# Kernel tuning notes

Hardware: AMD Instinct MI355X
Metric: run time of the kernel (lower is better)

The kernel has to match this reference:

```python
import jax, jax.numpy as jnp
import numpy as np
import math

EPS = 1e-5  # torch BatchNorm2d default eps
EXPANSION_RATE = 2


def _bn_train(x, gamma, beta):
    # BatchNorm2d in training mode: biased batch statistics over (B, H, W)
    mu = jnp.mean(x, axis=(0, 2, 3), keepdims=True)
    var = jnp.var(x, axis=(0, 2, 3), keepdims=True)
    xn = (x - mu) * jax.lax.rsqrt(var + EPS)
    return gamma[None, :, None, None] * xn + beta[None, :, None, None]


def _conv1x1(x, w, b):
    # w: [O, C]  (1x1 conv kernel squeezed), b: [O]
    return jnp.einsum('bchw,oc->bohw', x, w) + b[None, :, None, None]


def _lsgc(x, w_diff, b_diff, g_bn, be_bn, w_in, b_in, g_ibn, be_ibn,
          w_mr, b_mr, g_mbn, be_mbn):
    B, C, H, W = x.shape
    bit_depth = max(math.ceil(math.log2(H)), math.ceil(math.log2(W)))
    steps = [EXPANSION_RATE * 2 ** (n - 1) for n in range(1, bit_depth + 1)]

    fmax = None
    for step in steps:
        for axis, size in ((3, W), (2, H)):
            s = step % size
            for sgn in (1, -1):  # forward / backward rolls
                shifted = jnp.roll(x, sgn * s, axis=axis) if s else x
                d = x - shifted
                fmax = d if fmax is None else jnp.maximum(fmax, d)

    x_diff = _bn_train(_conv1x1(fmax, w_diff, b_diff), g_bn, be_bn)
    x_proc = _bn_train(_conv1x1(x, w_in, b_in), g_ibn, be_ibn)

    # MRConv: concat -> 1x1 conv -> BN -> GELU (exact) -> residual add
    x_cat = jnp.concatenate([x_proc, x_diff], axis=1)
    h = _bn_train(_conv1x1(x_cat, w_mr, b_mr), g_mbn, be_mbn)
    h = jax.nn.gelu(h, approximate=False)
    return x_proc + h


def setup_inputs() -> dict:
    key = jax.random.key(0)
    ks = jax.random.split(key, 8)
    B, C_in, C_out, H, W = 32, 128, 128, 64, 64

    def kaiming(k, o, i):
        return jax.random.normal(k, (o, i), jnp.float32) * np.sqrt(2.0 / i)

    return {
        'x': jax.random.normal(ks[0], (B, C_in, H, W), jnp.float32),
        'w_diff': kaiming(ks[1], C_out, C_in),
        'b_diff': jnp.zeros((C_out,), jnp.float32),
        'g_bn': jnp.ones((C_out,), jnp.float32),
        'be_bn': jnp.zeros((C_out,), jnp.float32),
        'w_in': kaiming(ks[2], C_out, C_in),
        'b_in': jnp.zeros((C_out,), jnp.float32),
        'g_ibn': jnp.ones((C_out,), jnp.float32),
        'be_ibn': jnp.zeros((C_out,), jnp.float32),
        'w_mr': kaiming(ks[3], C_out, 2 * C_out),
        'b_mr': jnp.zeros((C_out,), jnp.float32),
        'g_mbn': jnp.ones((C_out,), jnp.float32),
        'be_mbn': jnp.zeros((C_out,), jnp.float32),
    }


def reference(x, w_diff, b_diff, g_bn, be_bn, w_in, b_in, g_ibn, be_ibn,
              w_mr, b_mr, g_mbn, be_mbn):
    return _lsgc(x, w_diff, b_diff, g_bn, be_bn, w_in, b_in, g_ibn, be_ibn,
                 w_mr, b_mr, g_mbn, be_mbn)
```

## Files before the change

### kernel.cpp

```cpp
#include <hip/hip_runtime.h>
#include <math.h>


#define INV_NPIX (1.0f / 131072.0f)
#define EPS 1e-5f
#define KP 66
#define T1 4
#define T2 2

typedef __attribute__((ext_vector_type(8))) short s16x8;
typedef __attribute__((ext_vector_type(4))) float f32x4;

__device__ __forceinline__ uint32_t bf16_rne(float v) {
  uint32_t x = __float_as_uint(v);
  return (x + 0x7fffu + ((x >> 16) & 1u)) >> 16;
}
__device__ __forceinline__ uint32_t pack_hl(float v) {
  uint32_t h = bf16_rne(v);
  float lo = v - __uint_as_float(h << 16);
  return h | (bf16_rne(lo) << 16);
}
__device__ __forceinline__ float bf_lo(uint32_t d) {
  return __uint_as_float(d << 16);
}
__device__ __forceinline__ float bf_hi(uint32_t d) {
  return __uint_as_float(d & 0xffff0000u);
}
__device__ __forceinline__ float4 fmin4(float4 a, float4 b) {
  return make_float4(fminf(a.x, b.x), fminf(a.y, b.y), fminf(a.z, b.z),
                     fminf(a.w, b.w));
}

__global__ __launch_bounds__(256) void stencil_prep_kernel(
    const float* __restrict__ x, uint32_t* __restrict__ xp,
    uint32_t* __restrict__ fp, const float* __restrict__ w_in,
    const float* __restrict__ w_diff, unsigned short* __restrict__ wInH,
    unsigned short* __restrict__ wInL, unsigned short* __restrict__ wDfH,
    unsigned short* __restrict__ wDfL) {
  __shared__ float4 pA[1024];
  __shared__ float4 pB[1024];
  if (blockIdx.x >= 2048) {
    const int t = (blockIdx.x - 2048) * 256 + threadIdx.x;
    const int e = t & 16383;
    const float* w = (t < 16384) ? w_in : w_diff;
    unsigned short* aH = (t < 16384) ? wInH : wDfH;
    unsigned short* aL = (t < 16384) ? wInL : wDfL;
    const int j = e & 7, l = (e >> 3) & 63, mt = (e >> 9) & 7, kc = e >> 12;
    const int m = mt * 16 + (l & 15);
    const int k = kc * 32 + ((l >> 4) << 3) + j;
    const uint32_t p = pack_hl(w[m * 128 + k]);
    aH[e] = (unsigned short)(p & 0xffffu);
    aL[e] = (unsigned short)(p >> 16);
    return;
  }
  const int b = blockIdx.x >> 6;
  const int cp = blockIdx.x & 63;
  const float4* xa = (const float4*)x + (size_t)(b * 128 + 2 * cp) * 1024;
  const float4* xb = xa + 1024;
  float4 sA[4], sB[4];
#pragma unroll
  for (int i = 0; i < 4; ++i) {
    const int u = threadIdx.x + i * 256;
    sA[i] = xa[u];
    sB[i] = xb[u];
    pA[u] = sA[i];
    pB[u] = sB[i];
  }
  __syncthreads();
  const size_t obase = (size_t)(b * 64 + cp) * 1024;
#pragma unroll
  for (int i = 0; i < 4; ++i) {
    const int u = threadIdx.x + i * 256;
    const int h = u >> 4, wu = u & 15;
    const int row = u & ~15;
    float4 mA, mB;
    {
      const float4 A = sA[i];
      const float4 L = pA[row | ((wu + 15) & 15)];
      const float4 R = pA[row | ((wu + 1) & 15)];
      float4 m = fmin4(A, fmin4(L, R));
      m = fmin4(m, make_float4(A.z, A.w, R.x, R.y));
      m = fmin4(m, make_float4(L.z, L.w, A.x, A.y));
      m = fmin4(m, pA[row | ((wu + 2) & 15)]);
      m = fmin4(m, pA[row | ((wu + 14) & 15)]);
      m = fmin4(m, pA[row | ((wu + 4) & 15)]);
      m = fmin4(m, pA[row | ((wu + 12) & 15)]);
      m = fmin4(m, pA[row | ((wu + 8) & 15)]);
      m = fmin4(m, pA[(((h + 2) & 63) << 4) | wu]);
      m = fmin4(m, pA[(((h + 62) & 63) << 4) | wu]);
      m = fmin4(m, pA[(((h + 4) & 63) << 4) | wu]);
      m = fmin4(m, pA[(((h + 60) & 63) << 4) | wu]);
      m = fmin4(m, pA[(((h + 8) & 63) << 4) | wu]);
      m = fmin4(m, pA[(((h + 56) & 63) << 4) | wu]);
      m = fmin4(m, pA[(((h + 16) & 63) << 4) | wu]);
      m = fmin4(m, pA[(((h + 48) & 63) << 4) | wu]);
      m = fmin4(m, pA[(((h + 32) & 63) << 4) | wu]);
      mA = m;
    }
    {
      const float4 A = sB[i];
      const float4 L = pB[row | ((wu + 15) & 15)];
      const float4 R = pB[row | ((wu + 1) & 15)];
      float4 m = fmin4(A, fmin4(L, R));
      m = fmin4(m, make_float4(A.z, A.w, R.x, R.y));
      m = fmin4(m, make_float4(L.z, L.w, A.x, A.y));
      m = fmin4(m, pB[row | ((wu + 2) & 15)]);
      m = fmin4(m, pB[row | ((wu + 14) & 15)]);
      m = fmin4(m, pB[row | ((wu + 4) & 15)]);
      m = fmin4(m, pB[row | ((wu + 12) & 15)]);
      m = fmin4(m, pB[row | ((wu + 8) & 15)]);
      m = fmin4(m, pB[(((h + 2) & 63) << 4) | wu]);
      m = fmin4(m, pB[(((h + 62) & 63) << 4) | wu]);
      m = fmin4(m, pB[(((h + 4) & 63) << 4) | wu]);
      m = fmin4(m, pB[(((h + 60) & 63) << 4) | wu]);
      m = fmin4(m, pB[(((h + 8) & 63) << 4) | wu]);
      m = fmin4(m, pB[(((h + 56) & 63) << 4) | wu]);
      m = fmin4(m, pB[(((h + 16) & 63) << 4) | wu]);
      m = fmin4(m, pB[(((h + 48) & 63) << 4) | wu]);
      m = fmin4(m, pB[(((h + 32) & 63) << 4) | wu]);
      mB = m;
    }
    uint4 px, pf;
    px.x = bf16_rne(sA[i].x) | (bf16_rne(sB[i].x) << 16);
    px.y = bf16_rne(sA[i].y) | (bf16_rne(sB[i].y) << 16);
    px.z = bf16_rne(sA[i].z) | (bf16_rne(sB[i].z) << 16);
    px.w = bf16_rne(sA[i].w) | (bf16_rne(sB[i].w) << 16);
    pf.x = bf16_rne(sA[i].x - mA.x) | (bf16_rne(sB[i].x - mB.x) << 16);
    pf.y = bf16_rne(sA[i].y - mA.y) | (bf16_rne(sB[i].y - mB.y) << 16);
    pf.z = bf16_rne(sA[i].z - mA.z) | (bf16_rne(sB[i].z - mB.z) << 16);
    pf.w = bf16_rne(sA[i].w - mA.w) | (bf16_rne(sB[i].w - mB.w) << 16);
    ((uint4*)xp)[obase + u] = px;
    ((uint4*)fp)[obase + u] = pf;
  }
}

__device__ __forceinline__ void cwrite_stats(
    const f32x4 (&acc)[2][4], uint32_t* __restrict__ outp,
    float* __restrict__ pS, float* __restrict__ pQ, const int bx, const int b,
    const int hw0, const int wave, const int q, const int ln) {
#pragma unroll
  for (int mt2 = 0; mt2 < 2; ++mt2) {
    float sa[4] = {0.f, 0.f, 0.f, 0.f};
    float sq[4] = {0.f, 0.f, 0.f, 0.f};
#pragma unroll
    for (int nt = 0; nt < 4; ++nt) {
#pragma unroll
      for (int rp = 0; rp < 2; ++rp) {
        const float v0 = acc[mt2][nt][2 * rp];
        const float v1 = acc[mt2][nt][2 * rp + 1];
        const int m2 = (wave * 2 + mt2) * 8 + q * 2 + rp;
        outp[((size_t)(b * 64 + m2)) * 4096 + hw0 + nt * 16 + ln] =
            bf16_rne(v0) | (bf16_rne(v1) << 16);
        sa[2 * rp] += v0;
        sq[2 * rp] += v0 * v0;
        sa[2 * rp + 1] += v1;
        sq[2 * rp + 1] += v1 * v1;
      }
    }
#pragma unroll
    for (int off = 1; off < 16; off <<= 1) {
#pragma unroll
      for (int r = 0; r < 4; ++r) {
        sa[r] += __shfl_xor(sa[r], off);
        sq[r] += __shfl_xor(sq[r], off);
      }
    }
    if (ln == 0) {
#pragma unroll
      for (int r = 0; r < 4; ++r) {
        const int m = (wave * 2 + mt2) * 16 + q * 4 + r;
        pS[bx * 128 + m] = sa[r];
        pQ[bx * 128 + m] = sq[r];
      }
    }
  }
}

template <int T>
__device__ __forceinline__ void gemm1_persist(
    const unsigned short* __restrict__ AH, const unsigned short* __restrict__ AL,
    const uint32_t* __restrict__ B0, uint32_t* __restrict__ outp,
    float* __restrict__ pS, float* __restrict__ pQ, const int p,
    uint32_t* Bs) {
  const int tid = threadIdx.x;
  const int lane = tid & 63;
  const int wave = tid >> 6;
  const int sk2 = tid >> 4;
  const int sn4 = (tid & 15) << 2;
  const int q = lane >> 4;
  const int ln = lane & 15;

  uint4 ld[4];
  {
    const int bx0 = p * T;
    const int b = bx0 >> 6, hw0 = (bx0 & 63) << 6;
#pragma unroll
    for (int c = 0; c < 4; ++c)
      ld[c] = *(const uint4*)&B0[((size_t)(b * 64 + c * 16 + sk2)) * 4096 +
                                 hw0 + sn4];
  }

#pragma unroll
  for (int t = 0; t < T; ++t) {
    const int bx = p * T + t;
    const int b = bx >> 6, hw0 = (bx & 63) << 6;
    uint32_t* buf = Bs + (t & 1) * (64 * KP);

#pragma unroll
    for (int c = 0; c < 4; ++c)
      *(uint4*)&buf[(c * 16 + sk2) * KP + sn4] = ld[c];

    s16x8 ah[2][2], al[2][2];
#pragma unroll
    for (int mt2 = 0; mt2 < 2; ++mt2) {
      const size_t off = ((size_t)((wave * 2 + mt2) * 64 + lane)) << 3;
      ah[0][mt2] = *(const s16x8*)(AH + off);
      al[0][mt2] = *(const s16x8*)(AL + off);
    }
    __syncthreads();

    if (t + 1 < T) {
      const int bn = bx + 1;
      const int b2 = bn >> 6, hw2 = (bn & 63) << 6;
#pragma unroll
      for (int c = 0; c < 4; ++c)
        ld[c] = *(const uint4*)&B0[((size_t)(b2 * 64 + c * 16 + sk2)) * 4096 +
                                   hw2 + sn4];
    }

    f32x4 acc[2][4];
#pragma unroll
    for (int i = 0; i < 2; ++i)
#pragma unroll
      for (int j = 0; j < 4; ++j) acc[i][j] = (f32x4)(0.0f);

#pragma unroll
    for (int kc = 0; kc < 4; ++kc) {
      if (kc < 3) {
#pragma unroll
        for (int mt2 = 0; mt2 < 2; ++mt2) {
          const size_t off =
              ((size_t)(((kc + 1) * 8 + wave * 2 + mt2) * 64 + lane)) << 3;
          ah[(kc + 1) & 1][mt2] = *(const s16x8*)(AH + off);
          al[(kc + 1) & 1][mt2] = *(const s16x8*)(AL + off);
        }
      }
#pragma unroll
      for (int nt = 0; nt < 4; ++nt) {
        union { uint32_t u[4]; s16x8 s; } bb;
#pragma unroll
        for (int j = 0; j < 4; ++j)
          bb.u[j] = buf[(kc * 16 + q * 4 + j) * KP + nt * 16 + ln];
#pragma unroll
        for (int mt2 = 0; mt2 < 2; ++mt2) {
          acc[mt2][nt] = __builtin_amdgcn_mfma_f32_16x16x32_bf16(
              ah[kc & 1][mt2], bb.s, acc[mt2][nt], 0, 0, 0);
          acc[mt2][nt] = __builtin_amdgcn_mfma_f32_16x16x32_bf16(
              al[kc & 1][mt2], bb.s, acc[mt2][nt], 0, 0, 0);
        }
      }
    }

    cwrite_stats(acc, outp, pS, pQ, bx, b, hw0, wave, q, ln);
  }
}

__global__ __launch_bounds__(256) void gemm1_dual(
    const unsigned short* __restrict__ AH1, const unsigned short* __restrict__ AL1,
    const uint32_t* __restrict__ XP, uint32_t* __restrict__ out1,
    float* __restrict__ sv1, float* __restrict__ sq1,
    const unsigned short* __restrict__ AH2, const unsigned short* __restrict__ AL2,
    const uint32_t* __restrict__ FP, uint32_t* __restrict__ out2,
    float* __restrict__ sv2, float* __restrict__ sq2) {
  __shared__ uint32_t Bs[2 * 64 * KP];
  const int p = blockIdx.x & 511;
  if (blockIdx.x < 512)
    gemm1_persist<T1>(AH1, AL1, XP, out1, sv1, sq1, p, Bs);
  else
    gemm1_persist<T1>(AH2, AL2, FP, out2, sv2, sq2, p, Bs);
}

template <int T>
__device__ __forceinline__ void gemm2_persist(
    const unsigned short* __restrict__ AH, const unsigned short* __restrict__ AL,
    const uint32_t* __restrict__ B0, const uint32_t* __restrict__ B1,
    uint32_t* __restrict__ outp, float* __restrict__ pS,
    float* __restrict__ pQ, const int p, uint32_t* Bs) {
  const int tid = threadIdx.x;
  const int lane = tid & 63;
  const int wave = tid >> 6;
  const int sk2 = tid >> 4;
  const int sn4 = (tid & 15) << 2;
  const int q = lane >> 4;
  const int ln = lane & 15;

  uint4 ld[4];
  {
    const int bx0 = p * T;
    const int b = bx0 >> 6, hw0 = (bx0 & 63) << 6;
#pragma unroll
    for (int c = 0; c < 4; ++c)
      ld[c] = *(const uint4*)&B0[((size_t)(b * 64 + c * 16 + sk2)) * 4096 +
                                 hw0 + sn4];
  }

#pragma unroll
  for (int t = 0; t < T; ++t) {
    const int bx = p * T + t;
    const int b = bx >> 6, hw0 = (bx & 63) << 6;

    f32x4 acc[2][4];
#pragma unroll
    for (int i = 0; i < 2; ++i)
#pragma unroll
      for (int j = 0; j < 4; ++j) acc[i][j] = (f32x4)(0.0f);

    s16x8 ah[2][2], al[2][2];

    {
      uint32_t* buf = Bs;
#pragma unroll
      for (int c = 0; c < 4; ++c)
        *(uint4*)&buf[(c * 16 + sk2) * KP + sn4] = ld[c];
#pragma unroll
      for (int mt2 = 0; mt2 < 2; ++mt2) {
        const size_t off = ((size_t)((wave * 2 + mt2) * 64 + lane)) << 3;
        ah[0][mt2] = *(const s16x8*)(AH + off);
        al[0][mt2] = *(const s16x8*)(AL + off);
      }
      __syncthreads();
#pragma unroll
      for (int c = 0; c < 4; ++c)
        ld[c] = *(const uint4*)&B1[((size_t)(b * 64 + c * 16 + sk2)) * 4096 +
                                   hw0 + sn4];
#pragma unroll
      for (int kc = 0; kc < 4; ++kc) {
        if (kc < 3) {
#pragma unroll
          for (int mt2 = 0; mt2 < 2; ++mt2) {
            const size_t off =
                ((size_t)(((kc + 1) * 8 + wave * 2 + mt2) * 64 + lane)) << 3;
            ah[(kc + 1) & 1][mt2] = *(const s16x8*)(AH + off);
            al[(kc + 1) & 1][mt2] = *(const s16x8*)(AL + off);
          }
        }
#pragma unroll
        for (int nt = 0; nt < 4; ++nt) {
          union { uint32_t u[4]; s16x8 s; } bb;
#pragma unroll
          for (int j = 0; j < 4; ++j)
            bb.u[j] = buf[(kc * 16 + q * 4 + j) * KP + nt * 16 + ln];
#pragma unroll
          for (int mt2 = 0; mt2 < 2; ++mt2) {
            acc[mt2][nt] = __builtin_amdgcn_mfma_f32_16x16x32_bf16(
                ah[kc & 1][mt2], bb.s, acc[mt2][nt], 0, 0, 0);
            acc[mt2][nt] = __builtin_amdgcn_mfma_f32_16x16x32_bf16(
                al[kc & 1][mt2], bb.s, acc[mt2][nt], 0, 0, 0);
          }
        }
      }
    }

    {
      uint32_t* buf = Bs + 64 * KP;
#pragma unroll
      for (int c = 0; c < 4; ++c)
        *(uint4*)&buf[(c * 16 + sk2) * KP + sn4] = ld[c];
#pragma unroll
      for (int mt2 = 0; mt2 < 2; ++mt2) {
        const size_t off =
            ((size_t)((4 * 8 + wave * 2 + mt2) * 64 + lane)) << 3;
        ah[0][mt2] = *(const s16x8*)(AH + off);
        al[0][mt2] = *(const s16x8*)(AL + off);
      }
      __syncthreads();
      if (t + 1 < T) {
        const int bn = bx + 1;
        const int b2 = bn >> 6, hw2 = (bn & 63) << 6;
#pragma unroll
        for (int c = 0; c < 4; ++c)
          ld[c] = *(const uint4*)&B0[((size_t)(b2 * 64 + c * 16 + sk2)) * 4096 +
                                     hw2 + sn4];
      }
#pragma unroll
      for (int kc = 4; kc < 8; ++kc) {
        if (kc < 7) {
#pragma unroll
          for (int mt2 = 0; mt2 < 2; ++mt2) {
            const size_t off =
                ((size_t)(((kc + 1) * 8 + wave * 2 + mt2) * 64 + lane)) << 3;
            ah[(kc + 1) & 1][mt2] = *(const s16x8*)(AH + off);
            al[(kc + 1) & 1][mt2] = *(const s16x8*)(AL + off);
          }
        }
#pragma unroll
        for (int nt = 0; nt < 4; ++nt) {
          union { uint32_t u[4]; s16x8 s; } bb;
#pragma unroll
          for (int j = 0; j < 4; ++j)
            bb.u[j] = buf[((kc - 4) * 16 + q * 4 + j) * KP + nt * 16 + ln];
#pragma unroll
          for (int mt2 = 0; mt2 < 2; ++mt2) {
            acc[mt2][nt] = __builtin_amdgcn_mfma_f32_16x16x32_bf16(
                ah[kc & 1][mt2], bb.s, acc[mt2][nt], 0, 0, 0);
            acc[mt2][nt] = __builtin_amdgcn_mfma_f32_16x16x32_bf16(
                al[kc & 1][mt2], bb.s, acc[mt2][nt], 0, 0, 0);
          }
        }
      }
    }

    cwrite_stats(acc, outp, pS, pQ, bx, b, hw0, wave, q, ln);
  }
}

__global__ __launch_bounds__(256) void gemm2_kernel(
    const unsigned short* __restrict__ AH, const unsigned short* __restrict__ AL,
    const uint32_t* __restrict__ B0, const uint32_t* __restrict__ B1,
    uint32_t* __restrict__ outp, float* __restrict__ sv,
    float* __restrict__ sq) {
  __shared__ uint32_t Bs[2 * 64 * KP];
  gemm2_persist<T2>(AH, AL, B0, B1, outp, sv, sq, blockIdx.x, Bs);
}

__global__ __launch_bounds__(256) void reduce_kernel(
    const float* __restrict__ P, float* __restrict__ p2) {
  const int a = blockIdx.x >> 4, g = blockIdx.x & 15;
  const int c = threadIdx.x & 127, h = threadIdx.x >> 7;
  const float* src = P + ((size_t)(a * 2048 + g * 128 + h * 64)) * 128 + c;
  float s0 = 0.f, s1 = 0.f, s2 = 0.f, s3 = 0.f;
#pragma unroll
  for (int j = 0; j < 64; j += 4) {
    s0 += src[(j + 0) * 128];
    s1 += src[(j + 1) * 128];
    s2 += src[(j + 2) * 128];
    s3 += src[(j + 3) * 128];
  }
  __shared__ float sm[256];
  sm[threadIdx.x] = (s0 + s1) + (s2 + s3);
  __syncthreads();
  if (h == 0) p2[(a * 16 + g) * 128 + c] = sm[c] + sm[128 + c];
}

__global__ __launch_bounds__(256) void finalize1_kernel(
    const float* __restrict__ p2, const float* __restrict__ g_ibn,
    const float* __restrict__ be_ibn, const float* __restrict__ g_bn,
    const float* __restrict__ w_mr, float* __restrict__ a_in,
    float* __restrict__ d_in, unsigned short* __restrict__ wEffH,
    unsigned short* __restrict__ wEffL) {
  __shared__ float sa[256];
  const int t = threadIdx.x;
  if (t < 128) {
    float s = 0.f, qq = 0.f;
#pragma unroll
    for (int g = 0; g < 16; ++g) {
      s += p2[g * 128 + t];
      qq += p2[(16 + g) * 128 + t];
    }
    const float mu = s * INV_NPIX;
    const float var = fmaxf(qq * INV_NPIX - mu * mu, 0.f);
    const float a = g_ibn[t] * rsqrtf(var + EPS);
    if (blockIdx.x == 0) {
      a_in[t] = a;
      d_in[t] = be_ibn[t] - mu * a;
    }
    sa[t] = a;
  } else {
    const int c = t - 128;
    float s = 0.f, qq = 0.f;
#pragma unroll
    for (int g = 0; g < 16; ++g) {
      s += p2[(32 + g) * 128 + c];
      qq += p2[(48 + g) * 128 + c];
    }
    const float mu = s * INV_NPIX;
    const float var = fmaxf(qq * INV_NPIX - mu * mu, 0.f);
    sa[t] = g_bn[c] * rsqrtf(var + EPS);
  }
  __syncthreads();
  const int e = blockIdx.x * 256 + t;
  const int j = e & 7, l = (e >> 3) & 63, mt = (e >> 9) & 7, kc = e >> 12;
  const int m = mt * 16 + (l & 15);
  const int k = kc * 32 + ((l >> 4) << 3) + j;
  const uint32_t p = pack_hl(w_mr[m * 256 + k] * sa[k]);
  wEffH[e] = (unsigned short)(p & 0xffffu);
  wEffL[e] = (unsigned short)(p >> 16);
}

__global__ __launch_bounds__(128) void finalize2_kernel(
    const float* __restrict__ p2h, const float* __restrict__ g_mbn,
    const float* __restrict__ be_mbn, float* __restrict__ a_m,
    float* __restrict__ d_m) {
  const int t = threadIdx.x;
  float s = 0.f, qq = 0.f;
#pragma unroll
  for (int g = 0; g < 16; ++g) {
    s += p2h[g * 128 + t];
    qq += p2h[(16 + g) * 128 + t];
  }
  const float mu = s * INV_NPIX;
  const float var = fmaxf(qq * INV_NPIX - mu * mu, 0.f);
  const float a = g_mbn[t] * rsqrtf(var + EPS);
  a_m[t] = a;
  d_m[t] = be_mbn[t] - mu * a;
}

__device__ __forceinline__ float gelu_exact(float z) {
  return 0.5f * z * (1.0f + erff(z * 0.70710678118654752f));
}

__global__ __launch_bounds__(256) void epilogue_kernel(
    const uint32_t* __restrict__ yp, const uint32_t* __restrict__ hp,
    const float* __restrict__ a_in, const float* __restrict__ d_in,
    const float* __restrict__ a_m, const float* __restrict__ d_m,
    float* __restrict__ out) {
  const size_t i = (size_t)blockIdx.x * 256 + threadIdx.x;
  const int cp = (int)((i >> 10) & 63);
  const int b = (int)(i >> 16);
  const int c0 = 2 * cp, c1 = 2 * cp + 1;
  const uint4 yv = ((const uint4*)yp)[i];
  const uint4 hv = ((const uint4*)hp)[i];
  const float a0 = a_in[c0], d0 = d_in[c0], m0 = a_m[c0], e0 = d_m[c0];
  const float a1 = a_in[c1], d1 = d_in[c1], m1 = a_m[c1], e1 = d_m[c1];
  float4 o0, o1;
  o0.x = fmaf(a0, bf_lo(yv.x), d0) + gelu_exact(fmaf(m0, bf_lo(hv.x), e0));
  o0.y = fmaf(a0, bf_lo(yv.y), d0) + gelu_exact(fmaf(m0, bf_lo(hv.y), e0));
  o0.z = fmaf(a0, bf_lo(yv.z), d0) + gelu_exact(fmaf(m0, bf_lo(hv.z), e0));
  o0.w = fmaf(a0, bf_lo(yv.w), d0) + gelu_exact(fmaf(m0, bf_lo(hv.w), e0));
  o1.x = fmaf(a1, bf_hi(yv.x), d1) + gelu_exact(fmaf(m1, bf_hi(hv.x), e1));
  o1.y = fmaf(a1, bf_hi(yv.y), d1) + gelu_exact(fmaf(m1, bf_hi(hv.y), e1));
  o1.z = fmaf(a1, bf_hi(yv.z), d1) + gelu_exact(fmaf(m1, bf_hi(hv.z), e1));
  o1.w = fmaf(a1, bf_hi(yv.w), d1) + gelu_exact(fmaf(m1, bf_hi(hv.w), e1));
  const size_t u = i & 1023;
  ((float4*)out)[(size_t)(b * 128 + c0) * 1024 + u] = o0;
  ((float4*)out)[(size_t)(b * 128 + c1) * 1024 + u] = o1;
}

extern "C" void kernel_launch(void* const* d_in, const int* in_sizes, int n_in,
                              void* d_out, int out_size, void* d_ws,
                              size_t ws_size, hipStream_t stream) {
  const float* x = (const float*)d_in[0];
  const float* w_diff = (const float*)d_in[1];
  const float* g_bn = (const float*)d_in[3];
  const float* w_in = (const float*)d_in[5];
  const float* g_ibn = (const float*)d_in[7];
  const float* be_ibn = (const float*)d_in[8];
  const float* w_mr = (const float*)d_in[9];
  const float* g_mbn = (const float*)d_in[11];
  const float* be_mbn = (const float*)d_in[12];
  float* out = (float*)d_out;

  const size_t PD = (size_t)8388608;
  uint32_t* ws = (uint32_t*)d_ws;
  uint32_t* xp = ws;
  uint32_t* fpx = ws + PD;
  uint32_t* ypIn = ws + 2 * PD;
  uint32_t* ypDf = ws + 3 * PD;
  uint32_t* hp = ws + 4 * PD;
  float* st = (float*)(ws + 5 * PD);
  float* p2 = st;
  float* p2h = st + 8192;
  float* a_in = st + 12288, *dinc = st + 12416;
  float* a_m = st + 12544, *d_m = st + 12672;
  unsigned short* fr = (unsigned short*)(st + 12800);
  unsigned short* wInH = fr;
  unsigned short* wInL = fr + 16384;
  unsigned short* wDfH = fr + 32768;
  unsigned short* wDfL = fr + 49152;
  unsigned short* wEffH = fr + 65536;
  unsigned short* wEffL = fr + 98304;
  float* g1p = (float*)(ws + 4 * PD);
  float* g2p = (float*)ws;

  stencil_prep_kernel<<<2176, 256, 0, stream>>>(x, xp, fpx, w_in, w_diff,
                                                wInH, wInL, wDfH, wDfL);
  gemm1_dual<<<1024, 256, 0, stream>>>(wInH, wInL, xp, ypIn, g1p,
                                       g1p + 262144, wDfH, wDfL, fpx, ypDf,
                                       g1p + 524288, g1p + 786432);
  reduce_kernel<<<64, 256, 0, stream>>>(g1p, p2);
  finalize1_kernel<<<128, 256, 0, stream>>>(p2, g_ibn, be_ibn, g_bn, w_mr,
                                            a_in, dinc, wEffH, wEffL);
  gemm2_kernel<<<1024, 256, 0, stream>>>(wEffH, wEffL, ypIn, ypDf, hp, g2p,
                                         g2p + 262144);
  reduce_kernel<<<32, 256, 0, stream>>>(g2p, p2h);
  finalize2_kernel<<<1, 128, 0, stream>>>(p2h, g_mbn, be_mbn, a_m, d_m);
  epilogue_kernel<<<8192, 256, 0, stream>>>(ypIn, hp, a_in, dinc, a_m, d_m,
                                            out);
}
```

Measured before the change: 253.4 us.

## Stage GEMM tiles via direct global-to-LDS loads with XOR swizzle, defer stats writes

The GEMM kernels now stage B tiles with global_load_lds straight into an XOR-swizzled, unpadded LDS double buffer instead of round-tripping through registers. Accumulators are double-buffered so the previous tile's output and stats write overlaps the next tile's MFMA work. gemm2's two K halves are unified into one pipelined loop. The finalize2 kernel is folded into the epilogue, which now computes the BN coefficients per block and processes four chunks per thread, removing one launch. This costs extra accumulator registers and redundant per-block coefficient math.

Result: faster. 241.8 us (-4.6%).

```diff
diff --git a/kernel.cpp b/kernel.cpp
--- a/kernel.cpp
+++ b/kernel.cpp
@@ -4,7 +4,6 @@
 
 #define INV_NPIX (1.0f / 131072.0f)
 #define EPS 1e-5f
-#define KP 66
 #define T1 4
 #define T2 2
 
@@ -134,10 +133,28 @@
   }
 }
 
+__device__ __forceinline__ void stage_tile(const uint32_t* __restrict__ B,
+                                           const int b, const int hw0,
+                                           uint32_t* lbuf, const int wave,
+                                           const int lane) {
+  const int qq = lane >> 4, ln = lane & 15;
+#pragma unroll
+  for (int i = 0; i < 4; ++i) {
+    const int row = wave * 16 + i * 4 + qq;
+    const uint32_t* src =
+        &B[((size_t)(b * 64 + row)) * 4096 + hw0 + ((ln * 4) ^ (i << 4))];
+    uint32_t* dst = lbuf + (wave * 16 + i * 4) * 64;
+    __builtin_amdgcn_global_load_lds(
+        (const __attribute__((address_space(1))) void*)src,
+        (__attribute__((address_space(3))) void*)dst, 16, 0, 0);
+  }
+}
+
 __device__ __forceinline__ void cwrite_stats(
     const f32x4 (&acc)[2][4], uint32_t* __restrict__ outp,
-    float* __restrict__ pS, float* __restrict__ pQ, const int bx, const int b,
-    const int hw0, const int wave, const int q, const int ln) {
+    float* __restrict__ pS, float* __restrict__ pQ, const int bx,
+    const int wave, const int q, const int ln) {
+  const int b = bx >> 6, hw0 = (bx & 63) << 6;
 #pragma unroll
   for (int mt2 = 0; mt2 < 2; ++mt2) {
     float sa[4] = {0.f, 0.f, 0.f, 0.f};
@@ -185,31 +202,23 @@
   const int tid = threadIdx.x;
   const int lane = tid & 63;
   const int wave = tid >> 6;
-  const int sk2 = tid >> 4;
-  const int sn4 = (tid & 15) << 2;
   const int q = lane >> 4;
   const int ln = lane & 15;
 
-  uint4 ld[4];
-  {
-    const int bx0 = p * T;
-    const int b = bx0 >> 6, hw0 = (bx0 & 63) << 6;
-#pragma unroll
-    for (int c = 0; c < 4; ++c)
-      ld[c] = *(const uint4*)&B0[((size_t)(b * 64 + c * 16 + sk2)) * 4096 +
-                                 hw0 + sn4];
-  }
+  stage_tile(B0, (p * T) >> 6, ((p * T) & 63) << 6, Bs, wave, lane);
+
+  f32x4 accA[2][4], accB[2][4];
 
 #pragma unroll
   for (int t = 0; t < T; ++t) {
     const int bx = p * T + t;
-    const int b = bx >> 6, hw0 = (bx & 63) << 6;
-    uint32_t* buf = Bs + (t & 1) * (64 * KP);
-
-#pragma unroll
-    for (int c = 0; c < 4; ++c)
-      *(uint4*)&buf[(c * 16 + sk2) * KP + sn4] = ld[c];
-
+    uint32_t* buf = Bs + (t & 1) * 4096;
+    __syncthreads();
+    if (t + 1 < T) {
+      const int bn = bx + 1;
+      stage_tile(B0, bn >> 6, (bn & 63) << 6, Bs + ((t + 1) & 1) * 4096, wave,
+                 lane);
+    }
     s16x8 ah[2][2], al[2][2];
 #pragma unroll
     for (int mt2 = 0; mt2 < 2; ++mt2) {
@@ -217,23 +226,13 @@
       ah[0][mt2] = *(const s16x8*)(AH + off);
       al[0][mt2] = *(const s16x8*)(AL + off);
     }
-    __syncthreads();
-
-    if (t + 1 < T) {
-      const int bn = bx + 1;
-      const int b2 = bn >> 6, hw2 = (bn & 63) << 6;
-#pragma unroll
-      for (int c = 0; c < 4; ++c)
-        ld[c] = *(const uint4*)&B0[((size_t)(b2 * 64 + c * 16 + sk2)) * 4096 +
-                                   hw2 + sn4];
-    }
-
-    f32x4 acc[2][4];
+    if (t > 0)
+      cwrite_stats((t & 1) ? accA : accB, outp, pS, pQ, bx - 1, wave, q, ln);
+    f32x4(&acc)[2][4] = (t & 1) ? accB : accA;
 #pragma unroll
     for (int i = 0; i < 2; ++i)
 #pragma unroll
-      for (int j = 0; j < 4; ++j) acc[i][j] = (f32x4)(0.0f);
-
+      for (int jj = 0; jj < 4; ++jj) acc[i][jj] = (f32x4)(0.0f);
 #pragma unroll
     for (int kc = 0; kc < 4; ++kc) {
       if (kc < 3) {
@@ -250,7 +249,8 @@
         union { uint32_t u[4]; s16x8 s; } bb;
 #pragma unroll
         for (int j = 0; j < 4; ++j)
-          bb.u[j] = buf[(kc * 16 + q * 4 + j) * KP + nt * 16 + ln];
+          bb.u[j] =
+              buf[(kc * 16 + q * 4 + j) * 64 + ((nt * 16 + ln) ^ (q << 4))];
 #pragma unroll
         for (int mt2 = 0; mt2 < 2; ++mt2) {
           acc[mt2][nt] = __builtin_amdgcn_mfma_f32_16x16x32_bf16(
@@ -260,9 +260,9 @@
         }
       }
     }
-
-    cwrite_stats(acc, outp, pS, pQ, bx, b, hw0, wave, q, ln);
-  }
+  }
+  cwrite_stats(((T - 1) & 1) ? accB : accA, outp, pS, pQ, p * T + T - 1, wave,
+               q, ln);
 }
 
 __global__ __launch_bounds__(256) void gemm1_dual(
@@ -272,7 +272,7 @@
     const unsigned short* __restrict__ AH2, const unsigned short* __restrict__ AL2,
     const uint32_t* __restrict__ FP, uint32_t* __restrict__ out2,
     float* __restrict__ sv2, float* __restrict__ sq2) {
-  __shared__ uint32_t Bs[2 * 64 * KP];
+  __shared__ uint32_t Bs[2 * 4096];
   const int p = blockIdx.x & 511;
   if (blockIdx.x < 512)
     gemm1_persist<T1>(AH1, AL1, XP, out1, sv1, sq1, p, Bs);
@@ -289,129 +289,74 @@
   const int tid = threadIdx.x;
   const int lane = tid & 63;
   const int wave = tid >> 6;
-  const int sk2 = tid >> 4;
-  const int sn4 = (tid & 15) << 2;
   const int q = lane >> 4;
   const int ln = lane & 15;
 
-  uint4 ld[4];
-  {
-    const int bx0 = p * T;
-    const int b = bx0 >> 6, hw0 = (bx0 & 63) << 6;
-#pragma unroll
-    for (int c = 0; c < 4; ++c)
-      ld[c] = *(const uint4*)&B0[((size_t)(b * 64 + c * 16 + sk2)) * 4096 +
-                                 hw0 + sn4];
-  }
-
-#pragma unroll
-  for (int t = 0; t < T; ++t) {
+  stage_tile(B0, (p * T) >> 6, ((p * T) & 63) << 6, Bs, wave, lane);
+
+  f32x4 accA[2][4], accB[2][4];
+
+#pragma unroll
+  for (int s = 0; s < 2 * T; ++s) {
+    const int t = s >> 1, half = s & 1;
     const int bx = p * T + t;
-    const int b = bx >> 6, hw0 = (bx & 63) << 6;
-
-    f32x4 acc[2][4];
-#pragma unroll
-    for (int i = 0; i < 2; ++i)
-#pragma unroll
-      for (int j = 0; j < 4; ++j) acc[i][j] = (f32x4)(0.0f);
-
+    uint32_t* buf = Bs + (s & 1) * 4096;
+    __syncthreads();
+    if (s + 1 < 2 * T) {
+      const int s2 = s + 1;
+      const int bx2 = p * T + (s2 >> 1);
+      stage_tile((s2 & 1) ? B1 : B0, bx2 >> 6, (bx2 & 63) << 6,
+                 Bs + (s2 & 1) * 4096, wave, lane);
+    }
+    const int kb = half * 4;
     s16x8 ah[2][2], al[2][2];
-
-    {
-      uint32_t* buf = Bs;
-#pragma unroll
-      for (int c = 0; c < 4; ++c)
-        *(uint4*)&buf[(c * 16 + sk2) * KP + sn4] = ld[c];
-#pragma unroll
-      for (int mt2 = 0; mt2 < 2; ++mt2) {
-        const size_t off = ((size_t)((wave * 2 + mt2) * 64 + lane)) << 3;
-        ah[0][mt2] = *(const s16x8*)(AH + off);
-        al[0][mt2] = *(const s16x8*)(AL + off);
-      }
-      __syncthreads();
-#pragma unroll
-      for (int c = 0; c < 4; ++c)
-        ld[c] = *(const uint4*)&B1[((size_t)(b * 64 + c * 16 + sk2)) * 4096 +
-                                   hw0 + sn4];
-#pragma unroll
-      for (int kc = 0; kc < 4; ++kc) {
-        if (kc < 3) {
-#pragma unroll
-          for (int mt2 = 0; mt2 < 2; ++mt2) {
-            const size_t off =
-                ((size_t)(((kc + 1) * 8 + wave * 2 + mt2) * 64 + lane)) << 3;
-            ah[(kc + 1) & 1][mt2] = *(const s16x8*)(AH + off);
-            al[(kc + 1) & 1][mt2] = *(const s16x8*)(AL + off);
-          }
+#pragma unroll
+    for (int mt2 = 0; mt2 < 2; ++mt2) {
+      const size_t off =
+          ((size_t)((kb * 8 + wave * 2 + mt2) * 64 + lane)) << 3;
+      ah[0][mt2] = *(const s16x8*)(AH + off);
+      al[0][mt2] = *(const s16x8*)(AL + off);
+    }
+    f32x4(&acc)[2][4] = (t & 1) ? accB : accA;
+    if (half == 0) {
+      if (t > 0)
+        cwrite_stats((t & 1) ? accA : accB, outp, pS, pQ, bx - 1, wave, q, ln);
+#pragma unroll
+      for (int i = 0; i < 2; ++i)
+#pragma unroll
+        for (int jj = 0; jj < 4; ++jj) acc[i][jj] = (f32x4)(0.0f);
+    }
+#pragma unroll
+    for (int kc = 0; kc < 4; ++kc) {
+      if (kc < 3) {
+#pragma unroll
+        for (int mt2 = 0; mt2 < 2; ++mt2) {
+          const size_t off =
+              ((size_t)(((kb + kc + 1) * 8 + wave * 2 + mt2) * 64 + lane))
+              << 3;
+          ah[(kc + 1) & 1][mt2] = *(const s16x8*)(AH + off);
+          al[(kc + 1) & 1][mt2] = *(const s16x8*)(AL + off);
         }
-#pragma unroll
-        for (int nt = 0; nt < 4; ++nt) {
-          union { uint32_t u[4]; s16x8 s; } bb;
-#pragma unroll
-          for (int j = 0; j < 4; ++j)
-            bb.u[j] = buf[(kc * 16 + q * 4 + j) * KP + nt * 16 + ln];
-#pragma unroll
-          for (int mt2 = 0; mt2 < 2; ++mt2) {
-            acc[mt2][nt] = __builtin_amdgcn_mfma_f32_16x16x32_bf16(
-                ah[kc & 1][mt2], bb.s, acc[mt2][nt], 0, 0, 0);
-            acc[mt2][nt] = __builtin_amdgcn_mfma_f32_16x16x32_bf16(
-                al[kc & 1][mt2], bb.s, acc[mt2][nt], 0, 0, 0);
-          }
+      }
+#pragma unroll
+      for (int nt = 0; nt < 4; ++nt) {
+        union { uint32_t u[4]; s16x8 s; } bb;
+#pragma unroll
+        for (int j = 0; j < 4; ++j)
+          bb.u[j] =
+              buf[(kc * 16 + q * 4 + j) * 64 + ((nt * 16 + ln) ^ (q << 4))];
+#pragma unroll
+        for (int mt2 = 0; mt2 < 2; ++mt2) {
+          acc[mt2][nt] = __builtin_amdgcn_mfma_f32_16x16x32_bf16(
+              ah[kc & 1][mt2], bb.s, acc[mt2][nt], 0, 0, 0);
+          acc[mt2][nt] = __builtin_amdgcn_mfma_f32_16x16x32_bf16(
+              al[kc & 1][mt2], bb.s, acc[mt2][nt], 0, 0, 0);
         }
       }
     }
-
-    {
-      uint32_t* buf = Bs + 64 * KP;
-#pragma unroll
-      for (int c = 0; c < 4; ++c)
-        *(uint4*)&buf[(c * 16 + sk2) * KP + sn4] = ld[c];
-#pragma unroll
-      for (int mt2 = 0; mt2 < 2; ++mt2) {
-        const size_t off =
-            ((size_t)((4 * 8 + wave * 2 + mt2) * 64 + lane)) << 3;
-        ah[0][mt2] = *(const s16x8*)(AH + off);
-        al[0][mt2] = *(const s16x8*)(AL + off);
-      }
-      __syncthreads();
-      if (t + 1 < T) {
-        const int bn = bx + 1;
-        const int b2 = bn >> 6, hw2 = (bn & 63) << 6;
-#pragma unroll
-        for (int c = 0; c < 4; ++c)
-          ld[c] = *(const uint4*)&B0[((size_t)(b2 * 64 + c * 16 + sk2)) * 4096 +
-                                     hw2 + sn4];
-      }
-#pragma unroll
-      for (int kc = 4; kc < 8; ++kc) {
-        if (kc < 7) {
-#pragma unroll
-          for (int mt2 = 0; mt2 < 2; ++mt2) {
-            const size_t off =
-                ((size_t)(((kc + 1) * 8 + wave * 2 + mt2) * 64 + lane)) << 3;
-            ah[(kc + 1) & 1][mt2] = *(const s16x8*)(AH + off);
-            al[(kc + 1) & 1][mt2] = *(const s16x8*)(AL + off);
-          }
-        }
-#pragma unroll
-        for (int nt = 0; nt < 4; ++nt) {
-          union { uint32_t u[4]; s16x8 s; } bb;
-#pragma unroll
-          for (int j = 0; j < 4; ++j)
-            bb.u[j] = buf[((kc - 4) * 16 + q * 4 + j) * KP + nt * 16 + ln];
-#pragma unroll
-          for (int mt2 = 0; mt2 < 2; ++mt2) {
-            acc[mt2][nt] = __builtin_amdgcn_mfma_f32_16x16x32_bf16(
-                ah[kc & 1][mt2], bb.s, acc[mt2][nt], 0, 0, 0);
-            acc[mt2][nt] = __builtin_amdgcn_mfma_f32_16x16x32_bf16(
-                al[kc & 1][mt2], bb.s, acc[mt2][nt], 0, 0, 0);
-          }
-        }
-      }
-    }
-
-    cwrite_stats(acc, outp, pS, pQ, bx, b, hw0, wave, q, ln);
-  }
+  }
+  cwrite_stats(((T - 1) & 1) ? accB : accA, outp, pS, pQ, p * T + T - 1, wave,
+               q, ln);
 }
 
 __global__ __launch_bounds__(256) void gemm2_kernel(
@@ -419,7 +364,7 @@
     const uint32_t* __restrict__ B0, const uint32_t* __restrict__ B1,
     uint32_t* __restrict__ outp, float* __restrict__ sv,
     float* __restrict__ sq) {
-  __shared__ uint32_t Bs[2 * 64 * KP];
+  __shared__ uint32_t Bs[2 * 4096];
   gemm2_persist<T2>(AH, AL, B0, B1, outp, sv, sq, blockIdx.x, Bs);
 }
 
@@ -487,24 +432,6 @@
   wEffL[e] = (unsigned short)(p >> 16);
 }
 
-__global__ __launch_bounds__(128) void finalize2_kernel(
-    const float* __restrict__ p2h, const float* __restrict__ g_mbn,
-    const float* __restrict__ be_mbn, float* __restrict__ a_m,
-    float* __restrict__ d_m) {
-  const int t = threadIdx.x;
-  float s = 0.f, qq = 0.f;
-#pragma unroll
-  for (int g = 0; g < 16; ++g) {
-    s += p2h[g * 128 + t];
-    qq += p2h[(16 + g) * 128 + t];
-  }
-  const float mu = s * INV_NPIX;
-  const float var = fmaxf(qq * INV_NPIX - mu * mu, 0.f);
-  const float a = g_mbn[t] * rsqrtf(var + EPS);
-  a_m[t] = a;
-  d_m[t] = be_mbn[t] - mu * a;
-}
-
 __device__ __forceinline__ float gelu_exact(float z) {
   return 0.5f * z * (1.0f + erff(z * 0.70710678118654752f));
 }
@@ -512,28 +439,49 @@
 __global__ __launch_bounds__(256) void epilogue_kernel(
     const uint32_t* __restrict__ yp, const uint32_t* __restrict__ hp,
     const float* __restrict__ a_in, const float* __restrict__ d_in,
-    const float* __restrict__ a_m, const float* __restrict__ d_m,
-    float* __restrict__ out) {
-  const size_t i = (size_t)blockIdx.x * 256 + threadIdx.x;
-  const int cp = (int)((i >> 10) & 63);
-  const int b = (int)(i >> 16);
-  const int c0 = 2 * cp, c1 = 2 * cp + 1;
-  const uint4 yv = ((const uint4*)yp)[i];
-  const uint4 hv = ((const uint4*)hp)[i];
-  const float a0 = a_in[c0], d0 = d_in[c0], m0 = a_m[c0], e0 = d_m[c0];
-  const float a1 = a_in[c1], d1 = d_in[c1], m1 = a_m[c1], e1 = d_m[c1];
-  float4 o0, o1;
-  o0.x = fmaf(a0, bf_lo(yv.x), d0) + gelu_exact(fmaf(m0, bf_lo(hv.x), e0));
-  o0.y = fmaf(a0, bf_lo(yv.y), d0) + gelu_exact(fmaf(m0, bf_lo(hv.y), e0));
-  o0.z = fmaf(a0, bf_lo(yv.z), d0) + gelu_exact(fmaf(m0, bf_lo(hv.z), e0));
-  o0.w = fmaf(a0, bf_lo(yv.w), d0) + gelu_exact(fmaf(m0, bf_lo(hv.w), e0));
-  o1.x = fmaf(a1, bf_hi(yv.x), d1) + gelu_exact(fmaf(m1, bf_hi(hv.x), e1));
-  o1.y = fmaf(a1, bf_hi(yv.y), d1) + gelu_exact(fmaf(m1, bf_hi(hv.y), e1));
-  o1.z = fmaf(a1, bf_hi(yv.z), d1) + gelu_exact(fmaf(m1, bf_hi(hv.z), e1));
-  o1.w = fmaf(a1, bf_hi(yv.w), d1) + gelu_exact(fmaf(m1, bf_hi(hv.w), e1));
-  const size_t u = i & 1023;
-  ((float4*)out)[(size_t)(b * 128 + c0) * 1024 + u] = o0;
-  ((float4*)out)[(size_t)(b * 128 + c1) * 1024 + u] = o1;
+    const float* __restrict__ p2h, const float* __restrict__ g_mbn,
+    const float* __restrict__ be_mbn, float* __restrict__ out) {
+  __shared__ float sAi[128], sDi[128], sAm[128], sDm[128];
+  const int tid = threadIdx.x;
+  if (tid < 128) {
+    float s = 0.f, qq = 0.f;
+#pragma unroll
+    for (int g = 0; g < 16; ++g) {
+      s += p2h[g * 128 + tid];
+      qq += p2h[(16 + g) * 128 + tid];
+    }
+    const float mu = s * INV_NPIX;
+    const float var = fmaxf(qq * INV_NPIX - mu * mu, 0.f);
+    const float a = g_mbn[tid] * rsqrtf(var + EPS);
+    sAm[tid] = a;
+    sDm[tid] = be_mbn[tid] - mu * a;
+    sAi[tid] = a_in[tid];
+    sDi[tid] = d_in[tid];
+  }
+  __syncthreads();
+#pragma unroll
+  for (int it = 0; it < 4; ++it) {
+    const size_t i = (size_t)(blockIdx.x * 4 + it) * 256 + tid;
+    const int cp = (int)((i >> 10) & 63);
+    const int b = (int)(i >> 16);
+    const int c0 = 2 * cp, c1 = 2 * cp + 1;
+    const uint4 yv = ((const uint4*)yp)[i];
+    const uint4 hv = ((const uint4*)hp)[i];
+    const float a0 = sAi[c0], d0 = sDi[c0], m0 = sAm[c0], e0 = sDm[c0];
+    const float a1 = sAi[c1], d1 = sDi[c1], m1 = sAm[c1], e1 = sDm[c1];
+    float4 o0, o1;
+    o0.x = fmaf(a0, bf_lo(yv.x), d0) + gelu_exact(fmaf(m0, bf_lo(hv.x), e0));
+    o0.y = fmaf(a0, bf_lo(yv.y), d0) + gelu_exact(fmaf(m0, bf_lo(hv.y), e0));
+    o0.z = fmaf(a0, bf_lo(yv.z), d0) + gelu_exact(fmaf(m0, bf_lo(hv.z), e0));
+    o0.w = fmaf(a0, bf_lo(yv.w), d0) + gelu_exact(fmaf(m0, bf_lo(hv.w), e0));
+    o1.x = fmaf(a1, bf_hi(yv.x), d1) + gelu_exact(fmaf(m1, bf_hi(hv.x), e1));
+    o1.y = fmaf(a1, bf_hi(yv.y), d1) + gelu_exact(fmaf(m1, bf_hi(hv.y), e1));
+    o1.z = fmaf(a1, bf_hi(yv.z), d1) + gelu_exact(fmaf(m1, bf_hi(hv.z), e1));
+    o1.w = fmaf(a1, bf_hi(yv.w), d1) + gelu_exact(fmaf(m1, bf_hi(hv.w), e1));
+    const size_t u = i & 1023;
+    ((float4*)out)[(size_t)(b * 128 + c0) * 1024 + u] = o0;
+    ((float4*)out)[(size_t)(b * 128 + c1) * 1024 + u] = o1;
+  }
 }
 
 extern "C" void kernel_launch(void* const* d_in, const int* in_sizes, int n_in,
@@ -561,7 +509,6 @@
   float* p2 = st;
   float* p2h = st + 8192;
   float* a_in = st + 12288, *dinc = st + 12416;
-  float* a_m = st + 12544, *d_m = st + 12672;
   unsigned short* fr = (unsigned short*)(st + 12800);
   unsigned short* wInH = fr;
   unsigned short* wInL = fr + 16384;
@@ -583,7 +530,6 @@
   gemm2_kernel<<<1024, 256, 0, stream>>>(wEffH, wEffL, ypIn, ypDf, hp, g2p,
                                          g2p + 262144);
   reduce_kernel<<<32, 256, 0, stream>>>(g2p, p2h);
-  finalize2_kernel<<<1, 128, 0, stream>>>(p2h, g_mbn, be_mbn, a_m, d_m);
-  epilogue_kernel<<<8192, 256, 0, stream>>>(ypIn, hp, a_in, dinc, a_m, d_m,
-                                            out);
-}
+  epilogue_kernel<<<2048, 256, 0, stream>>>(ypIn, hp, a_in, dinc, p2h, g_mbn,
+                                            be_mbn, out);
+}
```
